# Kernel tuning notes

Hardware: AMD Instinct MI355X
Metric: run time of the kernel (lower is better)

The kernel has to match this reference:

```python
import jax, jax.numpy as jnp
import numpy as np

B, N, D, H = 4, 2048, 1024, 16
DH = D // H


def setup_inputs() -> dict:
    key = jax.random.key(0)
    ks = jax.random.split(key, 9)
    s = 1.0 / np.sqrt(D)
    return {
        "x": jax.random.normal(ks[0], (B, N, D), dtype=jnp.float32),
        "Wq": jax.random.normal(ks[1], (D, D), dtype=jnp.float32) * s,
        "bq": jax.random.normal(ks[2], (D,), dtype=jnp.float32) * 0.01,
        "Wk": jax.random.normal(ks[3], (D, D), dtype=jnp.float32) * s,
        "bk": jax.random.normal(ks[4], (D,), dtype=jnp.float32) * 0.01,
        "Wv": jax.random.normal(ks[5], (D, D), dtype=jnp.float32) * s,
        "bv": jax.random.normal(ks[6], (D,), dtype=jnp.float32) * 0.01,
        "Wp": jax.random.normal(ks[7], (D, D), dtype=jnp.float32) * s,
        "bp": jax.random.normal(ks[8], (D,), dtype=jnp.float32) * 0.01,
    }


def reference(x, Wq, bq, Wk, bk, Wv, bv, Wp, bp):
    b, n, d = x.shape
    # torch Linear: x @ W.T + b; reshape to (b, h, n, dh)
    def heads(W, bias):
        y = jnp.einsum('bnd,ed->bne', x, W) + bias
        return y.reshape(b, n, H, DH).transpose(0, 2, 1, 3)
    q, k, v = heads(Wq, bq), heads(Wk, bk), heads(Wv, bv)
    # NOTE: source multiplies by sqrt(d_head) (bug in original), kept faithfully
    scale = jnp.sqrt(jnp.float32(DH))
    att = jnp.einsum('bhqd,bhkd->bhqk', q, k) * scale
    causal = jnp.triu(jnp.ones((n, n), dtype=bool), k=1)  # True above diagonal
    att = jnp.where(causal, -jnp.inf, att)
    att = jax.nn.softmax(att, axis=-1)
    # dropout is eval-mode identity
    out = jnp.einsum('bhqk,bhkd->bhqd', att, v)
    out = out.transpose(0, 2, 1, 3).reshape(b, n, d)
    return jnp.einsum('bnd,ed->bne', out, Wp) + bp
```

## Files before the change

kernel.cpp:

```cpp
#include <hip/hip_runtime.h>
#include <hip/hip_fp16.h>


typedef _Float16 half8 __attribute__((ext_vector_type(8)));
typedef _Float16 half4 __attribute__((ext_vector_type(4)));
typedef float f32x4 __attribute__((ext_vector_type(4)));
typedef unsigned int u32x2 __attribute__((ext_vector_type(2)));

#define DEV __device__ __forceinline__
#define MFMA16(a, b, c) __builtin_amdgcn_mfma_f32_16x16x32_f16(a, b, c, 0, 0, 0)

DEV void gload_lds16(const void* g, void* l) {
  __builtin_amdgcn_global_load_lds(
      (const __attribute__((address_space(1))) void*)g,
      (__attribute__((address_space(3))) void*)l, 16, 0, 0);
}

__global__ __launch_bounds__(256) void cast_all(
    const float* __restrict__ x, const float* __restrict__ Wq,
    const float* __restrict__ Wk, const float* __restrict__ Wv,
    const float* __restrict__ Wp, __half* __restrict__ xb,
    __half* __restrict__ wqkv, __half* __restrict__ wpb) {
  int i = blockIdx.x * 256 + threadIdx.x;
  const float* s;
  __half* d;
  int j;
  if (i < 1048576) {
    s = x; d = xb; j = i;
  } else {
    int k = i - 1048576;
    int sel = k >> 17;
    j = k & 131071;
    s = (sel == 0) ? Wq : (sel == 1) ? Wk : (sel == 2) ? Wv : Wp;
    d = (sel == 3) ? wpb : (wqkv + sel * 1048576);
  }
  const float4* sp = (const float4*)s + (size_t)j * 2;
  float4 a = sp[0], b = sp[1];
  half8 h;
  h[0] = (_Float16)a.x; h[1] = (_Float16)a.y; h[2] = (_Float16)a.z; h[3] = (_Float16)a.w;
  h[4] = (_Float16)b.x; h[5] = (_Float16)b.y; h[6] = (_Float16)b.z; h[7] = (_Float16)b.w;
  *((half8*)d + j) = h;
}

__global__ __launch_bounds__(256, 2) void gemmQKV(
    const __half* __restrict__ A, const __half* __restrict__ Bm,
    const float* __restrict__ b0, const float* __restrict__ b1,
    const float* __restrict__ b2, __half* __restrict__ oh,
    __half* __restrict__ vtp) {
  const int n0 = blockIdx.x * 192;
  const int m0 = blockIdx.y * 128;
  const int tid = threadIdx.x;
  const int w = tid >> 6, lane = tid & 63;
  const int lr = lane & 15, lq = lane >> 4;
  const int wr = w >> 1, wc = w & 1;

  __shared__ alignas(16) __half As[2][8192];
  __shared__ alignas(16) __half Bs[2][12288];

  f32x4 acc[4][6] = {};

  const int srow = tid >> 3;
  const int scol = ((tid & 7) ^ (srow & 7)) * 8;
  const __half* Agp = A + ((size_t)m0 + srow) * 1024 + scol;
  const __half* Bgp = Bm + ((size_t)n0 + srow) * 1024 + scol;

#define STG(kt, buf)                                                           \
  do {                                                                         \
    const __half* ag = Agp + (kt)*64;                                          \
    const __half* bg = Bgp + (kt)*64;                                          \
    gload_lds16(ag, As[buf] + tid * 8);                                        \
    gload_lds16(ag + 32768, As[buf] + 2048 + tid * 8);                         \
    gload_lds16(ag + 65536, As[buf] + 4096 + tid * 8);                         \
    gload_lds16(ag + 98304, As[buf] + 6144 + tid * 8);                         \
    gload_lds16(bg, Bs[buf] + tid * 8);                                        \
    gload_lds16(bg + 32768, Bs[buf] + 2048 + tid * 8);                         \
    gload_lds16(bg + 65536, Bs[buf] + 4096 + tid * 8);                         \
    gload_lds16(bg + 98304, Bs[buf] + 6144 + tid * 8);                         \
    gload_lds16(bg + 131072, Bs[buf] + 8192 + tid * 8);                        \
    gload_lds16(bg + 163840, Bs[buf] + 10240 + tid * 8);                       \
  } while (0)

  STG(0, 0);
  asm volatile("" ::: "memory");

  for (int t = 0; t < 16; ++t) {
    const int s = t & 1;
    if (t < 15) {
      STG(t + 1, s ^ 1);
      asm volatile("s_waitcnt vmcnt(10)" ::: "memory");
    } else {
      asm volatile("s_waitcnt vmcnt(0)" ::: "memory");
    }
    __builtin_amdgcn_s_barrier();
    asm volatile("" ::: "memory");

    const char* Ac = (const char*)As[s];
    const char* Bc = (const char*)Bs[s];
    __builtin_amdgcn_s_setprio(1);
#pragma unroll
    for (int ks = 0; ks < 2; ++ks) {
      half8 af[4], bf[6];
#pragma unroll
      for (int mi = 0; mi < 4; ++mi) {
        int row = wr * 64 + mi * 16 + lr;
        af[mi] = *(const half8*)(Ac + ((row * 128 + ks * 64 + lq * 16) ^ ((row & 7) << 4)));
      }
#pragma unroll
      for (int ni = 0; ni < 6; ++ni) {
        int row = wc * 96 + ni * 16 + lr;
        bf[ni] = *(const half8*)(Bc + ((row * 128 + ks * 64 + lq * 16) ^ ((row & 7) << 4)));
      }
#pragma unroll
      for (int mi = 0; mi < 4; ++mi)
#pragma unroll
        for (int ni = 0; ni < 6; ++ni)
          acc[mi][ni] = MFMA16(af[mi], bf[ni], acc[mi][ni]);
    }
    __builtin_amdgcn_s_setprio(0);

    asm volatile("s_waitcnt lgkmcnt(0)" ::: "memory");
    __builtin_amdgcn_s_barrier();
    asm volatile("" ::: "memory");
  }

#pragma unroll
  for (int ni = 0; ni < 6; ++ni) {
    int col = n0 + wc * 96 + ni * 16 + lr;
    int t = col >> 10, e = col & 1023;
    const float* bb = (t == 0) ? b0 : ((t == 1) ? b1 : b2);
    float bias = bb[e];
    int hh = e >> 6, dh = e & 63;
    if (t == 2) {
#pragma unroll
      for (int mi = 0; mi < 4; ++mi) {
        int row = m0 + wr * 64 + mi * 16 + lq * 4;
        int b_ = row >> 11, n = row & 2047;
        half4 h;
#pragma unroll
        for (int r = 0; r < 4; ++r) h[r] = (_Float16)(acc[mi][ni][r] + bias);
        *(half4*)(vtp + (size_t)(b_ * 16 + hh) * 131072 + (size_t)dh * 2048 + n) = h;
      }
    } else {
      float scale = (t == 0) ? 11.541560327111707f : 1.0f;
      __half* base = oh + (size_t)t * 8388608 + dh;
#pragma unroll
      for (int mi = 0; mi < 4; ++mi)
#pragma unroll
        for (int r = 0; r < 4; ++r) {
          int row = m0 + wr * 64 + mi * 16 + lq * 4 + r;
          int b_ = row >> 11, n = row & 2047;
          float v = (acc[mi][ni][r] + bias) * scale;
          base[(((size_t)(b_ * 16 + hh) * 2048 + n) * 64)] = __float2half(v);
        }
    }
  }
#undef STG
}

__global__ __launch_bounds__(256) void gemm128p(
    const __half* __restrict__ A, const __half* __restrict__ Bm,
    const float* __restrict__ b0, float* __restrict__ of) {
  const int m0 = blockIdx.y * 128;
  const int n0 = blockIdx.x * 128;
  const int tid = threadIdx.x;
  const int w = tid >> 6, lane = tid & 63;
  const int lr = lane & 15, lq = lane >> 4;
  const int wr = w >> 1, wc = w & 1;

  __shared__ alignas(16) __half As[128 * 64];
  __shared__ alignas(16) __half Bs[128 * 64];

  f32x4 acc[4][4] = {};

  const int arow = lane >> 3;
  const int acol = ((lane & 7) ^ arow) * 8;
  const __half* Agp = A + ((size_t)m0 + w * 32 + arow) * 1024 + acol;
  const __half* Bgp = Bm + ((size_t)n0 + w * 32 + arow) * 1024 + acol;

  for (int kt = 0; kt < 16; ++kt) {
#pragma unroll
    for (int j = 0; j < 4; ++j) {
      gload_lds16(Agp + j * 8192 + kt * 64, As + (w * 4 + j) * 512);
      gload_lds16(Bgp + j * 8192 + kt * 64, Bs + (w * 4 + j) * 512);
    }
    __syncthreads();
#pragma unroll
    for (int s = 0; s < 2; ++s) {
      half8 af[4], bf[4];
#pragma unroll
      for (int i = 0; i < 4; ++i) {
        int rowA = wr * 64 + i * 16 + lr;
        int rowB = wc * 64 + i * 16 + lr;
        af[i] = *(const half8*)((const char*)As +
                                ((rowA * 128 + s * 64 + lq * 16) ^ ((rowA & 7) << 4)));
        bf[i] = *(const half8*)((const char*)Bs +
                                ((rowB * 128 + s * 64 + lq * 16) ^ ((rowB & 7) << 4)));
      }
#pragma unroll
      for (int mi = 0; mi < 4; ++mi)
#pragma unroll
        for (int ni = 0; ni < 4; ++ni)
          acc[mi][ni] = MFMA16(af[mi], bf[ni], acc[mi][ni]);
    }
    __syncthreads();
  }

#pragma unroll
  for (int ni = 0; ni < 4; ++ni) {
    int col = n0 + wc * 64 + ni * 16 + lr;
    float bias = b0[col];
#pragma unroll
    for (int mi = 0; mi < 4; ++mi)
#pragma unroll
      for (int r = 0; r < 4; ++r) {
        int row = m0 + wr * 64 + mi * 16 + lq * 4 + r;
        of[(size_t)row * 1024 + col] = acc[mi][ni][r] + bias;
      }
  }
}

__global__ __launch_bounds__(256, 3) void attn128(const __half* __restrict__ Q,
                                                  const __half* __restrict__ K,
                                                  const __half* __restrict__ Vt,
                                                  __half* __restrict__ O) {
  const int wg = blockIdx.x;
  const int bh = wg & 63;
  const int qt = 15 - (wg >> 6);
  const int b = bh >> 4, h = bh & 15;
  const int tid = threadIdx.x;
  const int w = tid >> 6, lane = tid & 63;
  const int lr = lane & 15, lq = lane >> 4;

  __shared__ alignas(16) __half Ks[2][4096];
  __shared__ alignas(16) __half Vs[2][4096];
  __shared__ alignas(16) unsigned Pl[4][512];

  const __half* Kb = K + (size_t)bh * 131072;
  const __half* Vb = Vt + (size_t)bh * 131072;

  const int srow0 = tid >> 3;
  const int srow1 = srow0 + 32;
  const int scol = ((tid & 7) ^ (srow0 & 7)) * 8;

#define STAGE(t, buf)                                                          \
  do {                                                                         \
    gload_lds16(Kb + (size_t)((t)*64 + srow0) * 64 + scol, Ks[buf] + tid * 8); \
    gload_lds16(Kb + (size_t)((t)*64 + srow1) * 64 + scol,                     \
                Ks[buf] + 2048 + tid * 8);                                     \
    gload_lds16(Vb + (size_t)srow0 * 2048 + (t)*64 + scol, Vs[buf] + tid * 8); \
    gload_lds16(Vb + (size_t)srow1 * 2048 + (t)*64 + scol,                     \
                Vs[buf] + 2048 + tid * 8);                                     \
  } while (0)

  const int q0 = qt * 128;
  const int ktend = 2 * qt + 2;
  const int rmin = q0 + w * 32;
  const int myqa = rmin + lr;
  const int myqb = rmin + 16 + lr;

  const __half* Qpa = Q + ((size_t)bh * 2048 + rmin) * 64;
  half8 qf0a = *(const half8*)(Qpa + lr * 64 + lq * 8);
  half8 qf1a = *(const half8*)(Qpa + lr * 64 + 32 + lq * 8);
  half8 qf0b = *(const half8*)(Qpa + (16 + lr) * 64 + lq * 8);
  half8 qf1b = *(const half8*)(Qpa + (16 + lr) * 64 + 32 + lq * 8);

  f32x4 oacca[4] = {}, oaccb[4] = {};
  float ma = -INFINITY, la = 0.f, mb = -INFINITY, lb = 0.f;

  STAGE(0, 0);
  asm volatile("" ::: "memory");

  char* Pc = (char*)Pl[w];

  auto smgrp = [&](f32x4* sacc, float& m, float& l, int myq, int k0,
                   bool needmask, f32x4* oacc, half8& pa0, half8& pa1) {
    if (needmask) {
#pragma unroll
      for (int nt = 0; nt < 4; ++nt)
#pragma unroll
        for (int r = 0; r < 4; ++r) {
          int key = k0 + nt * 16 + lq * 4 + r;
          if (key > myq) sacc[nt][r] = -INFINITY;
        }
    }
    float rm = fmaxf(sacc[0][0], sacc[0][1]);
    rm = fmaxf(fmaxf(rm, sacc[0][2]), sacc[0][3]);
    rm = fmaxf(fmaxf(rm, sacc[1][0]), sacc[1][1]);
    rm = fmaxf(fmaxf(rm, sacc[1][2]), sacc[1][3]);
    rm = fmaxf(fmaxf(rm, sacc[2][0]), sacc[2][1]);
    rm = fmaxf(fmaxf(rm, sacc[2][2]), sacc[2][3]);
    rm = fmaxf(fmaxf(rm, sacc[3][0]), sacc[3][1]);
    rm = fmaxf(fmaxf(rm, sacc[3][2]), sacc[3][3]);
    rm = fmaxf(rm, __shfl_xor(rm, 16));
    rm = fmaxf(rm, __shfl_xor(rm, 32));
    if (__any(rm > m + 8.f)) {
      float mn = fmaxf(m, rm);
      float al = __builtin_amdgcn_exp2f(m - mn);
      m = mn;
      l *= al;
      float al4[4];
#pragma unroll
      for (int r = 0; r < 4; ++r) al4[r] = __shfl(al, lq * 4 + r);
#pragma unroll
      for (int dt = 0; dt < 4; ++dt)
#pragma unroll
        for (int r = 0; r < 4; ++r) oacc[dt][r] *= al4[r];
    }
    float ps = 0.f;
#pragma unroll
    for (int nt = 0; nt < 4; ++nt) {
      float p0 = __builtin_amdgcn_exp2f(sacc[nt][0] - m);
      float p1 = __builtin_amdgcn_exp2f(sacc[nt][1] - m);
      float p2 = __builtin_amdgcn_exp2f(sacc[nt][2] - m);
      float p3 = __builtin_amdgcn_exp2f(sacc[nt][3] - m);
      sacc[nt][0] = p0; sacc[nt][1] = p1;
      sacc[nt][2] = p2; sacc[nt][3] = p3;
      ps += (p0 + p1) + (p2 + p3);
    }
    l += ps;
#pragma unroll
    for (int nt = 0; nt < 4; ++nt) {
      __half2 pha = __floats2half2_rn(sacc[nt][0], sacc[nt][1]);
      __half2 phb = __floats2half2_rn(sacc[nt][2], sacc[nt][3]);
      u32x2 pw;
      pw[0] = *(unsigned*)&pha;
      pw[1] = *(unsigned*)&phb;
      *(u32x2*)(Pc + ((lr * 128 + nt * 32 + lq * 8) ^ ((lr & 7) << 4))) = pw;
    }
    pa0 = *(const half8*)(Pc + ((lr * 128 + lq * 16) ^ ((lr & 7) << 4)));
    pa1 = *(const half8*)(Pc + ((lr * 128 + 64 + lq * 16) ^ ((lr & 7) << 4)));
  };

  for (int kt = 0; kt < ktend; ++kt) {
    const int cur = kt & 1;
    const int k0 = kt * 64;
    if (kt + 1 < ktend) {
      STAGE(kt + 1, cur ^ 1);
      asm volatile("s_waitcnt vmcnt(4)" ::: "memory");
    } else {
      asm volatile("s_waitcnt vmcnt(0)" ::: "memory");
    }
    __builtin_amdgcn_s_barrier();
    asm volatile("" ::: "memory");

    const char* Kc = (const char*)Ks[cur];
    const char* Vc = (const char*)Vs[cur];
    if (k0 <= rmin + 31) {
      f32x4 sa[4] = {}, sb[4] = {};
      __builtin_amdgcn_s_setprio(1);
#pragma unroll
      for (int nt = 0; nt < 4; ++nt) {
        int row = nt * 16 + lr;
        half8 kb0 = *(const half8*)(Kc + ((row * 128 + lq * 16) ^ ((row & 7) << 4)));
        half8 kb1 = *(const half8*)(Kc + ((row * 128 + 64 + lq * 16) ^ ((row & 7) << 4)));
        sa[nt] = MFMA16(kb0, qf0a, sa[nt]);
        sa[nt] = MFMA16(kb1, qf1a, sa[nt]);
        sb[nt] = MFMA16(kb0, qf0b, sb[nt]);
        sb[nt] = MFMA16(kb1, qf1b, sb[nt]);
      }
      __builtin_amdgcn_s_setprio(0);

      half8 paa0, paa1, pab0, pab1;
      smgrp(sa, ma, la, myqa, k0, k0 + 63 > rmin, oacca, paa0, paa1);
      smgrp(sb, mb, lb, myqb, k0, k0 + 63 > rmin + 16, oaccb, pab0, pab1);

      __builtin_amdgcn_s_setprio(1);
#pragma unroll
      for (int dt = 0; dt < 4; ++dt) {
        int row = dt * 16 + lr;
        half8 vb0 = *(const half8*)(Vc + ((row * 128 + lq * 16) ^ ((row & 7) << 4)));
        half8 vb1 = *(const half8*)(Vc + ((row * 128 + 64 + lq * 16) ^ ((row & 7) << 4)));
        oacca[dt] = MFMA16(paa0, vb0, oacca[dt]);
        oacca[dt] = MFMA16(paa1, vb1, oacca[dt]);
        oaccb[dt] = MFMA16(pab0, vb0, oaccb[dt]);
        oaccb[dt] = MFMA16(pab1, vb1, oaccb[dt]);
      }
      __builtin_amdgcn_s_setprio(0);
    }
    asm volatile("s_waitcnt lgkmcnt(0)" ::: "memory");
    __builtin_amdgcn_s_barrier();
    asm volatile("" ::: "memory");
  }

  auto epi = [&](f32x4* oacc, float lpart, int grow) {
    float lt = lpart;
    lt += __shfl_xor(lt, 16);
    lt += __shfl_xor(lt, 32);
    float linv = 1.0f / lt;
    float inv4[4];
#pragma unroll
    for (int r = 0; r < 4; ++r) inv4[r] = __shfl(linv, lq * 4 + r);
    __half* Op = O + ((size_t)b * 2048 + rmin + grow) * 1024 + h * 64;
#pragma unroll
    for (int dt = 0; dt < 4; ++dt)
#pragma unroll
      for (int r = 0; r < 4; ++r)
        Op[(size_t)(lq * 4 + r) * 1024 + dt * 16 + lr] =
            __float2half(oacc[dt][r] * inv4[r]);
  };
  epi(oacca, la, 0);
  epi(oaccb, lb, 16);
#undef STAGE
}

extern "C" void kernel_launch(void* const* d_in, const int* in_sizes, int n_in,
                              void* d_out, int out_size, void* d_ws,
                              size_t ws_size, hipStream_t stream) {
  const float* x = (const float*)d_in[0];
  const float* Wq = (const float*)d_in[1];
  const float* bq = (const float*)d_in[2];
  const float* Wk = (const float*)d_in[3];
  const float* bk = (const float*)d_in[4];
  const float* Wv = (const float*)d_in[5];
  const float* bv = (const float*)d_in[6];
  const float* Wp = (const float*)d_in[7];
  const float* bp = (const float*)d_in[8];

  char* ws = (char*)d_ws;
  const size_t XB = 0;
  const size_t WQKV = XB + 16777216;
  const size_t WPB = WQKV + 6291456;
  const size_t QKV = WPB + 2097152;
  const size_t VT = QKV + 50331648;
  const size_t OB = VT + 16777216;

  __half* xb = (__half*)(ws + XB);
  __half* wqkv = (__half*)(ws + WQKV);
  __half* wpb = (__half*)(ws + WPB);
  __half* qkv = (__half*)(ws + QKV);
  __half* vt = (__half*)(ws + VT);
  __half* ob = (__half*)(ws + OB);

  cast_all<<<6144, 256, 0, stream>>>(x, Wq, Wk, Wv, Wp, xb, wqkv, wpb);

  gemmQKV<<<dim3(16, 64), 256, 0, stream>>>(xb, wqkv, bq, bk, bv, qkv, vt);
  attn128<<<dim3(1024), 256, 0, stream>>>(qkv, qkv + 8388608, vt, ob);
  gemm128p<<<dim3(8, 64), 256, 0, stream>>>(ob, wpb, bp, (float*)d_out);
}
```

Measured before the change: 166.8 us.

## Single-buffer QKV GEMM LDS tiles to allow three blocks per CU

Replaces the double-buffered LDS staging in the QKV projection GEMM with a single buffer and raises the launch-bounds occupancy hint from 2 to 3 blocks. The next tile's load is now issued only after compute finishes and the barrier passes, so each block no longer overlaps its own loads with MFMA work. The intent is to hide memory latency across more resident blocks instead of within a block, at the cost of in-block pipelining and tighter register limits that may cause spills.

```diff
diff --git a/kernel.cpp b/kernel.cpp
--- a/kernel.cpp
+++ b/kernel.cpp
@@ -42,7 +42,7 @@
   *((half8*)d + j) = h;
 }
 
-__global__ __launch_bounds__(256, 2) void gemmQKV(
+__global__ __launch_bounds__(256, 3) void gemmQKV(
     const __half* __restrict__ A, const __half* __restrict__ Bm,
     const float* __restrict__ b0, const float* __restrict__ b1,
     const float* __restrict__ b2, __half* __restrict__ oh,
@@ -54,8 +54,8 @@
   const int lr = lane & 15, lq = lane >> 4;
   const int wr = w >> 1, wc = w & 1;
 
-  __shared__ alignas(16) __half As[2][8192];
-  __shared__ alignas(16) __half Bs[2][12288];
+  __shared__ alignas(16) __half As[8192];
+  __shared__ alignas(16) __half Bs[12288];
 
   f32x4 acc[4][6] = {};
 
@@ -64,38 +64,32 @@
   const __half* Agp = A + ((size_t)m0 + srow) * 1024 + scol;
   const __half* Bgp = Bm + ((size_t)n0 + srow) * 1024 + scol;
 
-#define STG(kt, buf)                                                           \
+#define STG(kt)                                                                \
   do {                                                                         \
     const __half* ag = Agp + (kt)*64;                                          \
     const __half* bg = Bgp + (kt)*64;                                          \
-    gload_lds16(ag, As[buf] + tid * 8);                                        \
-    gload_lds16(ag + 32768, As[buf] + 2048 + tid * 8);                         \
-    gload_lds16(ag + 65536, As[buf] + 4096 + tid * 8);                         \
-    gload_lds16(ag + 98304, As[buf] + 6144 + tid * 8);                         \
-    gload_lds16(bg, Bs[buf] + tid * 8);                                        \
-    gload_lds16(bg + 32768, Bs[buf] + 2048 + tid * 8);                         \
-    gload_lds16(bg + 65536, Bs[buf] + 4096 + tid * 8);                         \
-    gload_lds16(bg + 98304, Bs[buf] + 6144 + tid * 8);                         \
-    gload_lds16(bg + 131072, Bs[buf] + 8192 + tid * 8);                        \
-    gload_lds16(bg + 163840, Bs[buf] + 10240 + tid * 8);                       \
+    gload_lds16(ag, As + tid * 8);                                             \
+    gload_lds16(ag + 32768, As + 2048 + tid * 8);                              \
+    gload_lds16(ag + 65536, As + 4096 + tid * 8);                              \
+    gload_lds16(ag + 98304, As + 6144 + tid * 8);                              \
+    gload_lds16(bg, Bs + tid * 8);                                             \
+    gload_lds16(bg + 32768, Bs + 2048 + tid * 8);                              \
+    gload_lds16(bg + 65536, Bs + 4096 + tid * 8);                              \
+    gload_lds16(bg + 98304, Bs + 6144 + tid * 8);                              \
+    gload_lds16(bg + 131072, Bs + 8192 + tid * 8);                             \
+    gload_lds16(bg + 163840, Bs + 10240 + tid * 8);                            \
   } while (0)
 
-  STG(0, 0);
+  STG(0);
   asm volatile("" ::: "memory");
 
   for (int t = 0; t < 16; ++t) {
-    const int s = t & 1;
-    if (t < 15) {
-      STG(t + 1, s ^ 1);
-      asm volatile("s_waitcnt vmcnt(10)" ::: "memory");
-    } else {
-      asm volatile("s_waitcnt vmcnt(0)" ::: "memory");
-    }
+    asm volatile("s_waitcnt vmcnt(0)" ::: "memory");
     __builtin_amdgcn_s_barrier();
     asm volatile("" ::: "memory");
 
-    const char* Ac = (const char*)As[s];
-    const char* Bc = (const char*)Bs[s];
+    const char* Ac = (const char*)As;
+    const char* Bc = (const char*)Bs;
     __builtin_amdgcn_s_setprio(1);
 #pragma unroll
     for (int ks = 0; ks < 2; ++ks) {
@@ -121,6 +115,7 @@
     asm volatile("s_waitcnt lgkmcnt(0)" ::: "memory");
     __builtin_amdgcn_s_barrier();
     asm volatile("" ::: "memory");
+    if (t + 1 < 16) STG(t + 1);
   }
 
 #pragma unroll
```

After: 167.4 us. About the same (+0.4%).

## Fuse fp32-to-fp16 cast of x into QKV GEMM staging

Applied to the files above, without the earlier changes.

Drops the separate cast of the activation x to fp16. The QKV GEMM now loads fp32 x tiles into registers, converts them, and writes fp16 into LDS, software-pipelined two k-steps ahead, while the weights still go through direct global-to-LDS loads. This removes a 16MB fp16 write and its reread. In exchange each GEMM block reads fp32 A data, twice the bytes, 16 times over across the N-blocks, and adds register pressure and VALU conversion work in the main loop.

```diff
diff --git a/kernel.cpp b/kernel.cpp
--- a/kernel.cpp
+++ b/kernel.cpp
@@ -16,24 +16,15 @@
       (__attribute__((address_space(3))) void*)l, 16, 0, 0);
 }
 
-__global__ __launch_bounds__(256) void cast_all(
-    const float* __restrict__ x, const float* __restrict__ Wq,
-    const float* __restrict__ Wk, const float* __restrict__ Wv,
-    const float* __restrict__ Wp, __half* __restrict__ xb,
+__global__ __launch_bounds__(256) void cast_w(
+    const float* __restrict__ Wq, const float* __restrict__ Wk,
+    const float* __restrict__ Wv, const float* __restrict__ Wp,
     __half* __restrict__ wqkv, __half* __restrict__ wpb) {
   int i = blockIdx.x * 256 + threadIdx.x;
-  const float* s;
-  __half* d;
-  int j;
-  if (i < 1048576) {
-    s = x; d = xb; j = i;
-  } else {
-    int k = i - 1048576;
-    int sel = k >> 17;
-    j = k & 131071;
-    s = (sel == 0) ? Wq : (sel == 1) ? Wk : (sel == 2) ? Wv : Wp;
-    d = (sel == 3) ? wpb : (wqkv + sel * 1048576);
-  }
+  int sel = i >> 17;
+  int j = i & 131071;
+  const float* s = (sel == 0) ? Wq : (sel == 1) ? Wk : (sel == 2) ? Wv : Wp;
+  __half* d = (sel == 3) ? wpb : (wqkv + sel * 1048576);
   const float4* sp = (const float4*)s + (size_t)j * 2;
   float4 a = sp[0], b = sp[1];
   half8 h;
@@ -43,7 +34,7 @@
 }
 
 __global__ __launch_bounds__(256, 2) void gemmQKV(
-    const __half* __restrict__ A, const __half* __restrict__ Bm,
+    const float* __restrict__ A, const __half* __restrict__ Bm,
     const float* __restrict__ b0, const float* __restrict__ b1,
     const float* __restrict__ b2, __half* __restrict__ oh,
     __half* __restrict__ vtp) {
@@ -61,17 +52,35 @@
 
   const int srow = tid >> 3;
   const int scol = ((tid & 7) ^ (srow & 7)) * 8;
-  const __half* Agp = A + ((size_t)m0 + srow) * 1024 + scol;
+  const float* Agp = A + ((size_t)m0 + srow) * 1024 + scol;
   const __half* Bgp = Bm + ((size_t)n0 + srow) * 1024 + scol;
 
-#define STG(kt, buf)                                                           \
+  f32x4 ar[8];
+
+#define ALOAD(kt)                                                              \
   do {                                                                         \
-    const __half* ag = Agp + (kt)*64;                                          \
+    _Pragma("unroll") for (int c = 0; c < 4; ++c) {                            \
+      const float* ap = Agp + (size_t)c * 32768 + (kt)*64;                     \
+      ar[2 * c] = *(const f32x4*)ap;                                           \
+      ar[2 * c + 1] = *(const f32x4*)(ap + 4);                                 \
+    }                                                                          \
+  } while (0)
+
+#define AWRITE(buf)                                                            \
+  do {                                                                         \
+    _Pragma("unroll") for (int c = 0; c < 4; ++c) {                            \
+      half8 h;                                                                 \
+      h[0] = (_Float16)ar[2 * c][0]; h[1] = (_Float16)ar[2 * c][1];            \
+      h[2] = (_Float16)ar[2 * c][2]; h[3] = (_Float16)ar[2 * c][3];            \
+      h[4] = (_Float16)ar[2 * c + 1][0]; h[5] = (_Float16)ar[2 * c + 1][1];    \
+      h[6] = (_Float16)ar[2 * c + 1][2]; h[7] = (_Float16)ar[2 * c + 1][3];    \
+      *(half8*)(As[buf] + c * 2048 + tid * 8) = h;                             \
+    }                                                                          \
+  } while (0)
+
+#define BSTG(kt, buf)                                                          \
+  do {                                                                         \
     const __half* bg = Bgp + (kt)*64;                                          \
-    gload_lds16(ag, As[buf] + tid * 8);                                        \
-    gload_lds16(ag + 32768, As[buf] + 2048 + tid * 8);                         \
-    gload_lds16(ag + 65536, As[buf] + 4096 + tid * 8);                         \
-    gload_lds16(ag + 98304, As[buf] + 6144 + tid * 8);                         \
     gload_lds16(bg, Bs[buf] + tid * 8);                                        \
     gload_lds16(bg + 32768, Bs[buf] + 2048 + tid * 8);                         \
     gload_lds16(bg + 65536, Bs[buf] + 4096 + tid * 8);                         \
@@ -80,17 +89,24 @@
     gload_lds16(bg + 163840, Bs[buf] + 10240 + tid * 8);                       \
   } while (0)
 
-  STG(0, 0);
+  ALOAD(0);
+  BSTG(0, 0);
+  asm volatile("s_waitcnt vmcnt(6)" ::: "memory");
+  AWRITE(0);
+  ALOAD(1);
   asm volatile("" ::: "memory");
 
   for (int t = 0; t < 16; ++t) {
     const int s = t & 1;
     if (t < 15) {
-      STG(t + 1, s ^ 1);
-      asm volatile("s_waitcnt vmcnt(10)" ::: "memory");
+      BSTG(t + 1, s ^ 1);
+      asm volatile("s_waitcnt vmcnt(6)" ::: "memory");
+      AWRITE(s ^ 1);
+      if (t + 2 < 16) ALOAD(t + 2);
     } else {
       asm volatile("s_waitcnt vmcnt(0)" ::: "memory");
     }
+    asm volatile("s_waitcnt lgkmcnt(0)" ::: "memory");
     __builtin_amdgcn_s_barrier();
     asm volatile("" ::: "memory");
 
@@ -154,7 +170,9 @@
         }
     }
   }
-#undef STG
+#undef ALOAD
+#undef AWRITE
+#undef BSTG
 }
 
 __global__ __launch_bounds__(256) void gemm128p(
@@ -417,23 +435,21 @@
   const float* bp = (const float*)d_in[8];
 
   char* ws = (char*)d_ws;
-  const size_t XB = 0;
-  const size_t WQKV = XB + 16777216;
+  const size_t WQKV = 0;
   const size_t WPB = WQKV + 6291456;
   const size_t QKV = WPB + 2097152;
   const size_t VT = QKV + 50331648;
   const size_t OB = VT + 16777216;
 
-  __half* xb = (__half*)(ws + XB);
   __half* wqkv = (__half*)(ws + WQKV);
   __half* wpb = (__half*)(ws + WPB);
   __half* qkv = (__half*)(ws + QKV);
   __half* vt = (__half*)(ws + VT);
   __half* ob = (__half*)(ws + OB);
 
-  cast_all<<<6144, 256, 0, stream>>>(x, Wq, Wk, Wv, Wp, xb, wqkv, wpb);
-
-  gemmQKV<<<dim3(16, 64), 256, 0, stream>>>(xb, wqkv, bq, bk, bv, qkv, vt);
+  cast_w<<<2048, 256, 0, stream>>>(Wq, Wk, Wv, Wp, wqkv, wpb);
+
+  gemmQKV<<<dim3(16, 64), 256, 0, stream>>>(x, wqkv, bq, bk, bv, qkv, vt);
   attn128<<<dim3(1024), 256, 0, stream>>>(qkv, qkv + 8388608, vt, ob);
   gemm128p<<<dim3(8, 64), 256, 0, stream>>>(ob, wpb, bp, (float*)d_out);
 }
```

Result: no change. 168.5 us (+1.0%).
